# Performance work log

Hardware: AMD Instinct MI355X
Metric: run time of the kernel (lower is better)

The kernel has to match this reference:

```python
import jax, jax.numpy as jnp
import numpy as np

B, C, S = 32, 24, 7          # batch, feature channels, spatial side
N = S * S                    # 49 objects
Q = 2472                     # question vector dim (2524 - 2*(C+2))
RN = 256                     # rn_size


def _coords():
    # coord_tensor: [N, 2], ([i//7, i%7]) / 6
    i = jnp.arange(N)
    return jnp.stack([i // S, i % S], axis=1).astype(jnp.float32) / (S - 1)


def setup_inputs() -> dict:
    key = jax.random.key(0)
    ks = jax.random.split(key, 8)
    sc = lambda fan_in: 1.0 / np.sqrt(fan_in)
    return {
        "x":   jax.random.normal(ks[0], (B, C, S, S), dtype=jnp.float32),
        "qst": jax.random.normal(ks[1], (B, Q), dtype=jnp.float32),
        "W1":  jax.random.normal(ks[2], (2 * (C + 2) + Q, RN), dtype=jnp.float32) * sc(2524),
        "b1":  jax.random.normal(ks[3], (RN,), dtype=jnp.float32) * sc(2524),
        "Wg":  jax.random.normal(ks[4], (RN, RN), dtype=jnp.float32) * sc(RN),
        "bg":  jax.random.normal(ks[5], (RN,), dtype=jnp.float32) * sc(RN),
        "Wf":  jax.random.normal(ks[6], (RN, RN), dtype=jnp.float32) * sc(RN),
        "bf":  jax.random.normal(ks[7], (RN,), dtype=jnp.float32) * sc(RN),
        "g_layers": 2,
        "f_layers": 2,
    }


def reference(x, qst, W1, b1, Wg, bg, Wf, bf, g_layers, f_layers):
    mb = x.shape[0]
    # [B, C, 7, 7] -> [B, N, C], then append 2-d coords -> [B, N, C+2]
    x_flat = x.reshape(mb, C, N).transpose(0, 2, 1)
    coord = jnp.broadcast_to(_coords()[None], (mb, N, 2))
    x_flat = jnp.concatenate([x_flat, coord], axis=2)            # [B, N, D], D = C+2
    D = x_flat.shape[-1]

    # x_i[:, p, q, :] = x_flat[:, q, :]
    x_i = jnp.broadcast_to(x_flat[:, None, :, :], (mb, N, N, D))
    # x_j[:, p, q, :] = concat(x_flat[:, p, :], qst)
    xj_feat = jnp.concatenate(
        [x_flat, jnp.broadcast_to(qst[:, None, :], (mb, N, Q))], axis=2)  # [B, N, D+Q]
    x_j = jnp.broadcast_to(xj_feat[:, :, None, :], (mb, N, N, D + Q))
    x_full = jnp.concatenate([x_i, x_j], axis=3)                 # [B, N, N, 2D+Q]

    # g: shared edge MLP (note: ModuleList([Linear]*n) shares one weight)
    h = jax.nn.relu(jnp.einsum('bpqd,dr->bpqr', x_full, W1) + b1)
    for _ in range(g_layers):
        h = jax.nn.relu(jnp.einsum('bpqr,rs->bpqs', h, Wg) + bg)
    x_g = h.sum(axis=(1, 2))                                     # [B, RN]

    # f MLP (also shared weight across its layers)
    x_f = x_g
    for _ in range(f_layers):
        x_f = jax.nn.relu(x_f @ Wf + bf)
    return x_f
```

## Files before the change

kernel.cpp:

```cpp
#include <hip/hip_runtime.h>

#define BB 32
#define CC 24
#define SSIDE 7
#define NN 49
#define DD 26
#define QQ 2472
#define RN 256
#define NPQ 2401
#define BM 64
#define NT2 38
#define NJ 24
#define KCH 103

typedef float  f32x4  __attribute__((ext_vector_type(4)));
typedef short  short8 __attribute__((ext_vector_type(8)));
typedef __bf16 bfv8   __attribute__((ext_vector_type(8)));

#define A2_OFF   0
#define BJ_OFF   (A2_OFF + BB*NN*RN)
#define WGT_OFF  (BJ_OFF + BB*NN*RN)
#define PART_OFF (WGT_OFF + 32768)
#define QV_OFF   (PART_OFF + BB*NT2*RN)

static __device__ __forceinline__ short f2bf(float f) {
    return __builtin_bit_cast(short, (__bf16)f);
}


__global__ __launch_bounds__(256) void k_prep(const float* __restrict__ x,
                                              const float* __restrict__ qst,
                                              const float* __restrict__ W1,
                                              const float* __restrict__ b1,
                                              const float* __restrict__ Wg,
                                              float* __restrict__ ws) {
    const int bid = blockIdx.x;
    if (bid < BB * NJ) {
        const int xcd = bid & 7, qq = bid >> 3;
        const int b = xcd + 8 * (qq & 3), j = qq >> 2;
        const int r = threadIdx.x;
        const int k0 = j * KCH;
        const float* q = qst + b * QQ + k0;
        const float* w = W1 + (2 * DD + k0) * RN + r;
        float acc = 0.f;
        #pragma unroll 4
        for (int k = 0; k < KCH; ++k)
            acc += q[k] * w[k * RN];
        ws[QV_OFF + (b * NJ + j) * RN + r] = acc;
    } else if (bid < BB * NJ + 16) {
        const int t = bid - BB * NJ;
        const int kt = (t >> 2) * 64, nt = (t & 3) * 64;
        const int tx = threadIdx.x & 63, ty = threadIdx.x >> 6;
        __shared__ short lds[64 * 65];
        short* wgt = (short*)(ws + WGT_OFF);
        #pragma unroll
        for (int i = 0; i < 16; ++i) {
            const int k = ty + i * 4;
            lds[tx * 65 + k] = f2bf(Wg[(kt + k) * RN + nt + tx]);
        }
        __syncthreads();
        #pragma unroll
        for (int i = 0; i < 16; ++i) {
            const int n = ty + i * 4;
            wgt[(nt + n) * RN + kt + tx] = lds[n * 65 + tx];
        }
    } else {
        const int u = bid - (BB * NJ + 16);
        const int xcd = u & 7, qq = u >> 3;
        const int b = xcd + 8 * (qq & 3), n = qq >> 2;
        const int r = threadIdx.x;
        float a2 = 0.f, bj = b1[r];
        #pragma unroll
        for (int d = 0; d < DD; ++d) {
            float xv;
            if (d < CC)            xv = x[(b * CC + d) * NN + n];
            else if (d == CC)      xv = (float)(n / SSIDE) * (1.0f / 6.0f);
            else                   xv = (float)(n % SSIDE) * (1.0f / 6.0f);
            a2 += xv * W1[d * RN + r];
            bj += xv * W1[(DD + d) * RN + r];
        }
        ws[A2_OFF + (b * NN + n) * RN + r] = a2;
        ws[BJ_OFF + (b * NN + n) * RN + r] = bj;
    }
}

__global__ __launch_bounds__(256) void k_g_mfma(const float* __restrict__ bg,
                                                float* __restrict__ ws) {
    const int bid = blockIdx.x;
    const int xcd = bid & 7, qq = bid >> 3;
    const int b = xcd + 8 * (qq & 3), bx = qq >> 2;
    const int tid = threadIdx.x;
    const int lane = tid & 63, w = tid >> 6;
    const int lo = lane & 15, hi = lane >> 4;
    const int brow0 = bx * BM;
    const float* A2 = ws + A2_OFF + b * NN * RN;
    const float* Bj = ws + BJ_OFF + b * NN * RN;
    const short* wgt = (const short*)(ws + WGT_OFF);

    __shared__ short8 hbuf[BM * 32];
    __shared__ float qvs[RN];
    short* hb = (short*)hbuf;

    {
        float qv = 0.f;
        #pragma unroll 4
        for (int j = 0; j < NJ; ++j)
            qv += ws[QV_OFF + (b * NJ + j) * RN + tid];
        qvs[tid] = qv;
    }
    __syncthreads();

    #pragma unroll
    for (int it = 0; it < 8; ++it) {
        const int cid = it * 256 + tid;
        const int row = cid >> 5, chunk = cid & 31;
        const int grow = brow0 + row;
        short8 v8 = (short8)0;
        if (grow < NPQ) {
            const int p = grow / NN, q = grow - p * NN;
            const float4 a0 = *(const float4*)(A2 + q * RN + chunk * 8);
            const float4 a1 = *(const float4*)(A2 + q * RN + chunk * 8 + 4);
            const float4 b0 = *(const float4*)(Bj + p * RN + chunk * 8);
            const float4 b1v = *(const float4*)(Bj + p * RN + chunk * 8 + 4);
            const float* qc = qvs + chunk * 8;
            v8[0] = f2bf(fmaxf(a0.x + b0.x + qc[0], 0.f));
            v8[1] = f2bf(fmaxf(a0.y + b0.y + qc[1], 0.f));
            v8[2] = f2bf(fmaxf(a0.z + b0.z + qc[2], 0.f));
            v8[3] = f2bf(fmaxf(a0.w + b0.w + qc[3], 0.f));
            v8[4] = f2bf(fmaxf(a1.x + b1v.x + qc[4], 0.f));
            v8[5] = f2bf(fmaxf(a1.y + b1v.y + qc[5], 0.f));
            v8[6] = f2bf(fmaxf(a1.z + b1v.z + qc[6], 0.f));
            v8[7] = f2bf(fmaxf(a1.w + b1v.w + qc[7], 0.f));
        }
        hbuf[row * 32 + (chunk ^ (row & 7))] = v8;
    }

    const int wcol0 = w * 64;
    bfv8 bfr[4][8];
    #pragma unroll
    for (int ct = 0; ct < 4; ++ct) {
        const int n = wcol0 + ct * 16 + lo;
        #pragma unroll
        for (int ks = 0; ks < 8; ++ks)
            bfr[ct][ks] = __builtin_bit_cast(bfv8,
                *(const short8*)(wgt + n * RN + ks * 32 + hi * 8));
    }
    float bgv[4];
    #pragma unroll
    for (int ct = 0; ct < 4; ++ct)
        bgv[ct] = bg[wcol0 + ct * 16 + lo];

    __syncthreads();

    f32x4 acc[4][4];

    #pragma unroll
    for (int ct = 0; ct < 4; ++ct)
        #pragma unroll
        for (int rt = 0; rt < 4; ++rt)
            acc[ct][rt] = (f32x4){0.f, 0.f, 0.f, 0.f};
    #pragma unroll
    for (int rt = 0; rt < 4; ++rt) {
        const int row = rt * 16 + lo;
        bfv8 afr[8];
        #pragma unroll
        for (int ks = 0; ks < 8; ++ks)
            afr[ks] = __builtin_bit_cast(bfv8,
                hbuf[row * 32 + ((ks * 4 + hi) ^ (row & 7))]);
        #pragma unroll
        for (int ct = 0; ct < 4; ++ct)
            #pragma unroll
            for (int ks = 0; ks < 8; ++ks)
                acc[ct][rt] = __builtin_amdgcn_mfma_f32_16x16x32_bf16(
                    afr[ks], bfr[ct][ks], acc[ct][rt], 0, 0, 0);
    }

    __syncthreads();
    #pragma unroll
    for (int ct = 0; ct < 4; ++ct) {
        const int n = wcol0 + ct * 16 + lo;
        #pragma unroll
        for (int rt = 0; rt < 4; ++rt) {
            #pragma unroll
            for (int r = 0; r < 4; ++r) {
                const int row = rt * 16 + hi * 4 + r;
                const float v = fmaxf(acc[ct][rt][r] + bgv[ct], 0.f);
                hb[row * 256 + (((n >> 3) ^ (row & 7)) << 3) + (n & 7)] = f2bf(v);
            }
        }
    }
    __syncthreads();

    #pragma unroll
    for (int ct = 0; ct < 4; ++ct)
        #pragma unroll
        for (int rt = 0; rt < 4; ++rt)
            acc[ct][rt] = (f32x4){0.f, 0.f, 0.f, 0.f};
    #pragma unroll
    for (int rt = 0; rt < 4; ++rt) {
        const int row = rt * 16 + lo;
        bfv8 afr[8];
        #pragma unroll
        for (int ks = 0; ks < 8; ++ks)
            afr[ks] = __builtin_bit_cast(bfv8,
                hbuf[row * 32 + ((ks * 4 + hi) ^ (row & 7))]);
        #pragma unroll
        for (int ct = 0; ct < 4; ++ct)
            #pragma unroll
            for (int ks = 0; ks < 8; ++ks)
                acc[ct][rt] = __builtin_amdgcn_mfma_f32_16x16x32_bf16(
                    afr[ks], bfr[ct][ks], acc[ct][rt], 0, 0, 0);
    }

    float cs[4] = {0.f, 0.f, 0.f, 0.f};
    #pragma unroll
    for (int ct = 0; ct < 4; ++ct) {
        #pragma unroll
        for (int rt = 0; rt < 4; ++rt) {
            #pragma unroll
            for (int r = 0; r < 4; ++r) {
                const int grow = brow0 + rt * 16 + hi * 4 + r;
                const float v = fmaxf(acc[ct][rt][r] + bgv[ct], 0.f);
                cs[ct] += (grow < NPQ) ? v : 0.f;
            }
        }
    }
    #pragma unroll
    for (int ct = 0; ct < 4; ++ct) {
        float v = cs[ct];
        v += __shfl_xor(v, 16);
        v += __shfl_xor(v, 32);
        if (hi == 0)
            ws[PART_OFF + (b * NT2 + bx) * RN + wcol0 + ct * 16 + lo] = v;
    }
}

__global__ void k_f_reduce(const float* __restrict__ Wf,
                           const float* __restrict__ bf,
                           const float* __restrict__ ws,
                           float* __restrict__ out) {
    const int b = blockIdx.x, r = threadIdx.x;
    __shared__ float xs[RN];
    float xg = 0.f;
    for (int t = 0; t < NT2; ++t)
        xg += ws[PART_OFF + (b * NT2 + t) * RN + r];
    xs[r] = xg;
    __syncthreads();

    float v = 0.f;
    #pragma unroll
    for (int layer = 0; layer < 2; ++layer) {
        float acc = bf[r];
        for (int s = 0; s < RN; ++s)
            acc += xs[s] * Wf[s * RN + r];
        v = fmaxf(acc, 0.f);
        __syncthreads();
        xs[r] = v;
        __syncthreads();
    }
    out[b * RN + r] = v;
}

extern "C" void kernel_launch(void* const* d_in, const int* in_sizes, int n_in,
                              void* d_out, int out_size, void* d_ws, size_t ws_size,
                              hipStream_t stream) {
    const float* x   = (const float*)d_in[0];
    const float* qst = (const float*)d_in[1];
    const float* W1  = (const float*)d_in[2];
    const float* b1  = (const float*)d_in[3];
    const float* Wg  = (const float*)d_in[4];
    const float* bg  = (const float*)d_in[5];
    const float* Wf  = (const float*)d_in[6];
    const float* bf  = (const float*)d_in[7];
    float* out = (float*)d_out;
    float* ws  = (float*)d_ws;

    k_prep      <<<BB * NJ + 16 + BB * NN, RN, 0, stream>>>(x, qst, W1, b1, Wg, ws);
    k_g_mfma    <<<NT2 * BB, RN, 0, stream>>>(bg, ws);
    k_f_reduce  <<<BB, RN, 0, stream>>>(Wf, bf, ws, out);
}
```

Measured before the change: 146.7 us.

## Make g-MLP kernel persistent per batch slice with double-buffered tile staging

```diff
diff --git a/kernel.cpp b/kernel.cpp
--- a/kernel.cpp
+++ b/kernel.cpp
@@ -10,6 +10,7 @@
 #define NPQ 2401
 #define BM 64
 #define NT2 38
+#define NSUB 16
 #define NJ 24
 #define KCH 103
 
@@ -21,7 +22,7 @@
 #define BJ_OFF   (A2_OFF + BB*NN*RN)
 #define WGT_OFF  (BJ_OFF + BB*NN*RN)
 #define PART_OFF (WGT_OFF + 32768)
-#define QV_OFF   (PART_OFF + BB*NT2*RN)
+#define QV_OFF   (PART_OFF + BB*NSUB*RN)
 
 static __device__ __forceinline__ short f2bf(float f) {
     return __builtin_bit_cast(short, (__bf16)f);
@@ -84,22 +85,21 @@
     }
 }
 
-__global__ __launch_bounds__(256) void k_g_mfma(const float* __restrict__ bg,
-                                                float* __restrict__ ws) {
+__global__ __launch_bounds__(256, 2) void k_g_mfma2(const float* __restrict__ bg,
+                                                    float* __restrict__ ws) {
     const int bid = blockIdx.x;
-    const int xcd = bid & 7, qq = bid >> 3;
-    const int b = xcd + 8 * (qq & 3), bx = qq >> 2;
+    const int xcd = bid & 7, q5 = bid >> 3;
+    const int b = xcd + 8 * (q5 & 3), sub = q5 >> 2;
     const int tid = threadIdx.x;
     const int lane = tid & 63, w = tid >> 6;
     const int lo = lane & 15, hi = lane >> 4;
-    const int brow0 = bx * BM;
     const float* A2 = ws + A2_OFF + b * NN * RN;
     const float* Bj = ws + BJ_OFF + b * NN * RN;
     const short* wgt = (const short*)(ws + WGT_OFF);
 
-    __shared__ short8 hbuf[BM * 32];
+    __shared__ short8 hbuf[2][BM * 32];
     __shared__ float qvs[RN];
-    short* hb = (short*)hbuf;
+    const int njobs = (NT2 - sub + NSUB - 1) / NSUB;
 
     {
         float qv = 0.f;
@@ -108,32 +108,6 @@
             qv += ws[QV_OFF + (b * NJ + j) * RN + tid];
         qvs[tid] = qv;
     }
-    __syncthreads();
-
-    #pragma unroll
-    for (int it = 0; it < 8; ++it) {
-        const int cid = it * 256 + tid;
-        const int row = cid >> 5, chunk = cid & 31;
-        const int grow = brow0 + row;
-        short8 v8 = (short8)0;
-        if (grow < NPQ) {
-            const int p = grow / NN, q = grow - p * NN;
-            const float4 a0 = *(const float4*)(A2 + q * RN + chunk * 8);
-            const float4 a1 = *(const float4*)(A2 + q * RN + chunk * 8 + 4);
-            const float4 b0 = *(const float4*)(Bj + p * RN + chunk * 8);
-            const float4 b1v = *(const float4*)(Bj + p * RN + chunk * 8 + 4);
-            const float* qc = qvs + chunk * 8;
-            v8[0] = f2bf(fmaxf(a0.x + b0.x + qc[0], 0.f));
-            v8[1] = f2bf(fmaxf(a0.y + b0.y + qc[1], 0.f));
-            v8[2] = f2bf(fmaxf(a0.z + b0.z + qc[2], 0.f));
-            v8[3] = f2bf(fmaxf(a0.w + b0.w + qc[3], 0.f));
-            v8[4] = f2bf(fmaxf(a1.x + b1v.x + qc[4], 0.f));
-            v8[5] = f2bf(fmaxf(a1.y + b1v.y + qc[5], 0.f));
-            v8[6] = f2bf(fmaxf(a1.z + b1v.z + qc[6], 0.f));
-            v8[7] = f2bf(fmaxf(a1.w + b1v.w + qc[7], 0.f));
-        }
-        hbuf[row * 32 + (chunk ^ (row & 7))] = v8;
-    }
 
     const int wcol0 = w * 64;
     bfv8 bfr[4][8];
@@ -152,86 +126,130 @@
 
     __syncthreads();
 
+    #define STAGE_TILE(TSTART, BUFI)                                           \
+    do {                                                                       \
+        const int brow0_ = (TSTART) * BM;                                      \
+        _Pragma("unroll")                                                      \
+        for (int it = 0; it < 8; ++it) {                                       \
+            const int cid = it * 256 + tid;                                    \
+            const int row = cid >> 5, chunk = cid & 31;                        \
+            const int grow = brow0_ + row;                                     \
+            short8 v8 = (short8)0;                                             \
+            if (grow < NPQ) {                                                  \
+                const int p = grow / NN, qo = grow - p * NN;                   \
+                const float4 a0 = *(const float4*)(A2 + qo * RN + chunk * 8);  \
+                const float4 a1 = *(const float4*)(A2 + qo * RN + chunk * 8 + 4);\
+                const float4 b0 = *(const float4*)(Bj + p * RN + chunk * 8);   \
+                const float4 b1v = *(const float4*)(Bj + p * RN + chunk * 8 + 4);\
+                const float* qc = qvs + chunk * 8;                             \
+                v8[0] = f2bf(fmaxf(a0.x + b0.x + qc[0], 0.f));                 \
+                v8[1] = f2bf(fmaxf(a0.y + b0.y + qc[1], 0.f));                 \
+                v8[2] = f2bf(fmaxf(a0.z + b0.z + qc[2], 0.f));                 \
+                v8[3] = f2bf(fmaxf(a0.w + b0.w + qc[3], 0.f));                 \
+                v8[4] = f2bf(fmaxf(a1.x + b1v.x + qc[4], 0.f));                \
+                v8[5] = f2bf(fmaxf(a1.y + b1v.y + qc[5], 0.f));                \
+                v8[6] = f2bf(fmaxf(a1.z + b1v.z + qc[6], 0.f));                \
+                v8[7] = f2bf(fmaxf(a1.w + b1v.w + qc[7], 0.f));                \
+            }                                                                  \
+            hbuf[BUFI][row * 32 + (chunk ^ (row & 7))] = v8;                   \
+        }                                                                      \
+    } while (0)
+
+    STAGE_TILE(sub, 0);
+    __syncthreads();
+
+    float cs[4] = {0.f, 0.f, 0.f, 0.f};
     f32x4 acc[4][4];
 
-    #pragma unroll
-    for (int ct = 0; ct < 4; ++ct)
-        #pragma unroll
-        for (int rt = 0; rt < 4; ++rt)
-            acc[ct][rt] = (f32x4){0.f, 0.f, 0.f, 0.f};
-    #pragma unroll
-    for (int rt = 0; rt < 4; ++rt) {
-        const int row = rt * 16 + lo;
-        bfv8 afr[8];
-        #pragma unroll
-        for (int ks = 0; ks < 8; ++ks)
-            afr[ks] = __builtin_bit_cast(bfv8,
-                hbuf[row * 32 + ((ks * 4 + hi) ^ (row & 7))]);
+    for (int i = 0; i < njobs; ++i) {
+        const int cur = i & 1;
+        const int tcur = sub + i * NSUB;
+        short8* hbc = hbuf[cur];
+        short* hb = (short*)hbc;
+
         #pragma unroll
         for (int ct = 0; ct < 4; ++ct)
             #pragma unroll
+            for (int rt = 0; rt < 4; ++rt)
+                acc[ct][rt] = (f32x4){0.f, 0.f, 0.f, 0.f};
+        #pragma unroll
+        for (int rt = 0; rt < 4; ++rt) {
+            const int row = rt * 16 + lo;
+            bfv8 afr[8];
+            #pragma unroll
             for (int ks = 0; ks < 8; ++ks)
-                acc[ct][rt] = __builtin_amdgcn_mfma_f32_16x16x32_bf16(
-                    afr[ks], bfr[ct][ks], acc[ct][rt], 0, 0, 0);
-    }
-
-    __syncthreads();
-    #pragma unroll
-    for (int ct = 0; ct < 4; ++ct) {
-        const int n = wcol0 + ct * 16 + lo;
+                afr[ks] = __builtin_bit_cast(bfv8,
+                    hbc[row * 32 + ((ks * 4 + hi) ^ (row & 7))]);
+            #pragma unroll
+            for (int ks = 0; ks < 8; ++ks)
+                #pragma unroll
+                for (int ct = 0; ct < 4; ++ct)
+                    acc[ct][rt] = __builtin_amdgcn_mfma_f32_16x16x32_bf16(
+                        afr[ks], bfr[ct][ks], acc[ct][rt], 0, 0, 0);
+        }
+        __syncthreads();
+
+        #pragma unroll
+        for (int ct = 0; ct < 4; ++ct) {
+            const int n = wcol0 + ct * 16 + lo;
+            #pragma unroll
+            for (int rt = 0; rt < 4; ++rt) {
+                #pragma unroll
+                for (int r = 0; r < 4; ++r) {
+                    const int row = rt * 16 + hi * 4 + r;
+                    const float v = fmaxf(acc[ct][rt][r] + bgv[ct], 0.f);
+                    hb[row * 256 + (((n >> 3) ^ (row & 7)) << 3) + (n & 7)] = f2bf(v);
+                }
+            }
+        }
+
+        if (i + 1 < njobs)
+            STAGE_TILE(tcur + NSUB, cur ^ 1);
+        __syncthreads();
+
+        #pragma unroll
+        for (int ct = 0; ct < 4; ++ct)
+            #pragma unroll
+            for (int rt = 0; rt < 4; ++rt)
+                acc[ct][rt] = (f32x4){0.f, 0.f, 0.f, 0.f};
         #pragma unroll
         for (int rt = 0; rt < 4; ++rt) {
-            #pragma unroll
-            for (int r = 0; r < 4; ++r) {
-                const int row = rt * 16 + hi * 4 + r;
-                const float v = fmaxf(acc[ct][rt][r] + bgv[ct], 0.f);
-                hb[row * 256 + (((n >> 3) ^ (row & 7)) << 3) + (n & 7)] = f2bf(v);
+            const int row = rt * 16 + lo;
+            bfv8 afr[8];
+            #pragma unroll
+            for (int ks = 0; ks < 8; ++ks)
+                afr[ks] = __builtin_bit_cast(bfv8,
+                    hbc[row * 32 + ((ks * 4 + hi) ^ (row & 7))]);
+            #pragma unroll
+            for (int ks = 0; ks < 8; ++ks)
+                #pragma unroll
+                for (int ct = 0; ct < 4; ++ct)
+                    acc[ct][rt] = __builtin_amdgcn_mfma_f32_16x16x32_bf16(
+                        afr[ks], bfr[ct][ks], acc[ct][rt], 0, 0, 0);
+        }
+        const int brow0 = tcur * BM;
+        #pragma unroll
+        for (int ct = 0; ct < 4; ++ct) {
+            #pragma unroll
+            for (int rt = 0; rt < 4; ++rt) {
+                #pragma unroll
+                for (int r = 0; r < 4; ++r) {
+                    const int grow = brow0 + rt * 16 + hi * 4 + r;
+                    const float v = fmaxf(acc[ct][rt][r] + bgv[ct], 0.f);
+                    cs[ct] += (grow < NPQ) ? v : 0.f;
+                }
             }
         }
     }
-    __syncthreads();
-
-    #pragma unroll
-    for (int ct = 0; ct < 4; ++ct)
-        #pragma unroll
-        for (int rt = 0; rt < 4; ++rt)
-            acc[ct][rt] = (f32x4){0.f, 0.f, 0.f, 0.f};
-    #pragma unroll
-    for (int rt = 0; rt < 4; ++rt) {
-        const int row = rt * 16 + lo;
-        bfv8 afr[8];
-        #pragma unroll
-        for (int ks = 0; ks < 8; ++ks)
-            afr[ks] = __builtin_bit_cast(bfv8,
-                hbuf[row * 32 + ((ks * 4 + hi) ^ (row & 7))]);
-        #pragma unroll
-        for (int ct = 0; ct < 4; ++ct)
-            #pragma unroll
-            for (int ks = 0; ks < 8; ++ks)
-                acc[ct][rt] = __builtin_amdgcn_mfma_f32_16x16x32_bf16(
-                    afr[ks], bfr[ct][ks], acc[ct][rt], 0, 0, 0);
-    }
-
-    float cs[4] = {0.f, 0.f, 0.f, 0.f};
-    #pragma unroll
-    for (int ct = 0; ct < 4; ++ct) {
-        #pragma unroll
-        for (int rt = 0; rt < 4; ++rt) {
-            #pragma unroll
-            for (int r = 0; r < 4; ++r) {
-                const int grow = brow0 + rt * 16 + hi * 4 + r;
-                const float v = fmaxf(acc[ct][rt][r] + bgv[ct], 0.f);
-                cs[ct] += (grow < NPQ) ? v : 0.f;
-            }
-        }
-    }
+    #undef STAGE_TILE
+
     #pragma unroll
     for (int ct = 0; ct < 4; ++ct) {
         float v = cs[ct];
         v += __shfl_xor(v, 16);
         v += __shfl_xor(v, 32);
         if (hi == 0)
-            ws[PART_OFF + (b * NT2 + bx) * RN + wcol0 + ct * 16 + lo] = v;
+            ws[PART_OFF + (b * NSUB + sub) * RN + wcol0 + ct * 16 + lo] = v;
     }
 }
 
@@ -242,8 +260,9 @@
     const int b = blockIdx.x, r = threadIdx.x;
     __shared__ float xs[RN];
     float xg = 0.f;
-    for (int t = 0; t < NT2; ++t)
-        xg += ws[PART_OFF + (b * NT2 + t) * RN + r];
+    #pragma unroll
+    for (int t = 0; t < NSUB; ++t)
+        xg += ws[PART_OFF + (b * NSUB + t) * RN + r];
     xs[r] = xg;
     __syncthreads();
 
@@ -276,6 +295,6 @@
     float* ws  = (float*)d_ws;
 
     k_prep      <<<BB * NJ + 16 + BB * NN, RN, 0, stream>>>(x, qst, W1, b1, Wg, ws);
-    k_g_mfma    <<<NT2 * BB, RN, 0, stream>>>(bg, ws);
+    k_g_mfma2   <<<NSUB * BB, RN, 0, stream>>>(bg, ws);
     k_f_reduce  <<<BB, RN, 0, stream>>>(Wf, bf, ws, out);
 }
```

Result: slower. 165.4 us (+12.7%).
